# Performance work log

Hardware: AMD Instinct MI355X
Metric: run time of the kernel (lower is better)

## Reference

```python
import jax, jax.numpy as jnp
import numpy as np

B, T, H = 4, 1024, 4096
N_Q, N_KV, HD = 32, 8, 128
N_REP = N_Q // N_KV
THETA = 10000.0


def setup_inputs() -> dict:
    key = jax.random.key(0)
    k0, k1, k2 = jax.random.split(key, 3)
    x = jax.random.normal(k0, (B, T, H), dtype=jnp.float32)
    w_qkv = jax.random.normal(k1, ((N_Q + 2 * N_KV) * HD, H), dtype=jnp.float32) * 0.02
    w_proj = jax.random.normal(k2, (N_Q * HD, H), dtype=jnp.float32).T * 0.02  # [H, N_Q*HD] -> stored as [out,in]=[4096,4096]
    # real RoPE frequencies, matching precompute_freqs_cis(theta=10000)
    inv_freq = 1.0 / (THETA ** (np.arange(0, HD, 2, dtype=np.float32) / HD))  # [HD/2]
    angles = np.arange(T, dtype=np.float32)[:, None] * inv_freq[None, :]      # [T, HD/2]
    freqs_cos = jnp.asarray(np.cos(angles))
    freqs_sin = jnp.asarray(np.sin(angles))
    return {"x": x, "w_qkv": w_qkv, "w_proj": w_proj,
            "freqs_cos": freqs_cos, "freqs_sin": freqs_sin}


def _rope(x, cos, sin):
    # x: [B, T, nH, HD]; consecutive pairs (x[2i], x[2i+1]) form complex numbers
    x0 = x[..., 0::2]
    x1 = x[..., 1::2]
    c = cos[None, :, None, :]
    s = sin[None, :, None, :]
    r0 = x0 * c - x1 * s
    r1 = x0 * s + x1 * c
    return jnp.stack([r0, r1], axis=-1).reshape(x.shape)


def reference(x, w_qkv, w_proj, freqs_cos, freqs_sin):
    q_per_kv = N_Q // N_KV
    qkv = jnp.einsum('bth,oh->bto', x, w_qkv)                 # [B,T,(N_Q+2*N_KV)*HD]
    qkv = qkv.reshape(B, T, N_KV, q_per_kv + 2, HD)           # interleaved GQA layout
    q = qkv[:, :, :, :q_per_kv, :].reshape(B, T, N_Q, HD)
    k = qkv[:, :, :, q_per_kv, :]                              # [B,T,N_KV,HD]
    v = qkv[:, :, :, q_per_kv + 1, :]
    q = _rope(q, freqs_cos, freqs_sin)
    k = _rope(k, freqs_cos, freqs_sin)
    k = jnp.repeat(k, N_REP, axis=2)                           # [B,T,N_Q,HD]
    v = jnp.repeat(v, N_REP, axis=2)
    q = q.transpose(0, 2, 1, 3)                                # [B,H,T,HD]
    k = k.transpose(0, 2, 1, 3)
    v = v.transpose(0, 2, 1, 3)
    scale = 1.0 / jnp.sqrt(jnp.float32(HD))
    scores = jnp.einsum('bhqd,bhkd->bhqk', q, k) * scale       # [B,H,T,T]
    causal = jnp.tril(jnp.ones((T, T), dtype=bool))
    scores = jnp.where(causal[None, None], scores, jnp.finfo(scores.dtype).min)
    attn = jax.nn.softmax(scores, axis=-1)
    out = jnp.einsum('bhqk,bhkd->bhqd', attn, v)               # [B,H,T,HD]
    out = out.transpose(0, 2, 1, 3).reshape(B, T, N_Q * HD)
    return jnp.einsum('bto,ho->bth', out, w_proj)              # RowParallel proj, [B,T,H]
```

## Files before the change

### kernel.cpp

```cpp
#include <hip/hip_runtime.h>
#include <cstddef>

#define DEVINL __device__ __forceinline__

typedef float f32x4 __attribute__((ext_vector_type(4)));
typedef __bf16 bf16x8 __attribute__((ext_vector_type(8)));

DEVINL unsigned short f2bf(float f) {
  union { float f; unsigned int u; } v; v.f = f;
  unsigned int u = v.u;
  unsigned int r = (u + 0x7fffu + ((u >> 16) & 1u)) >> 16;
  return (unsigned short)r;
}
DEVINL float bf2f(unsigned short s) {
  union { unsigned int u; float f; } v; v.u = ((unsigned int)s) << 16;
  return v.f;
}
DEVINL uint4 pack8(const unsigned short o[8]) {
  uint4 r;
  r.x = (unsigned int)o[0] | ((unsigned int)o[1] << 16);
  r.y = (unsigned int)o[2] | ((unsigned int)o[3] << 16);
  r.z = (unsigned int)o[4] | ((unsigned int)o[5] << 16);
  r.w = (unsigned int)o[6] | ((unsigned int)o[7] << 16);
  return r;
}
DEVINL void gload16(const void* g, void* l) {
  __builtin_amdgcn_global_load_lds(
      (__attribute__((address_space(1))) void*)g,
      (__attribute__((address_space(3))) void*)l, 16, 0, 0);
}

__global__ __launch_bounds__(256) void k_cvt(const float* __restrict__ in,
                                             unsigned short* __restrict__ out, int n4) {
  int i = blockIdx.x * 256 + threadIdx.x;
  if (i >= n4) return;
  float4 v = ((const float4*)in)[i];
  ushort4 o;
  o.x = f2bf(v.x); o.y = f2bf(v.y); o.z = f2bf(v.z); o.w = f2bf(v.w);
  ((ushort4*)out)[i] = o;
}

template <int OUT_BF16>
__global__ __launch_bounds__(512, 1) void k_gemm256(const unsigned short* __restrict__ A,
                                                    const unsigned short* __restrict__ Bt,
                                                    void* __restrict__ Cout,
                                                    int M, int N, int K) {
  __shared__ __align__(16) unsigned short As[2][2][256 * 32];
  __shared__ __align__(16) unsigned short Bs[2][2][256 * 32];
  const int t = threadIdx.x, lane = t & 63;
  const int wid = t >> 6, wm = wid >> 2, wn = wid & 3;
  const int fr = lane & 15, kq = lane >> 4;
  const int nwg = gridDim.x * gridDim.y;
  int lin = blockIdx.y * gridDim.x + blockIdx.x;
  lin = (lin & 7) * (nwg >> 3) + (lin >> 3);
  const int bx = lin % gridDim.x, by = lin / gridDim.x;
  const int row0 = by * 256, col0 = bx * 256;
  const int NT = K >> 6;

  int srow[2], sgs[2];
#pragma unroll
  for (int i = 0; i < 2; ++i) {
    const int off = (i * 512 + t) * 16;
    srow[i] = off >> 6;
    sgs[i] = (((off >> 4) & 3) - (srow[i] >> 1)) & 3;
  }

#define STAGE_A(KT, KS)                                                        \
  do {                                                                         \
    const int b_ = (KT) & 1;                                                   \
    _Pragma("unroll") for (int i = 0; i < 2; ++i)                              \
        gload16(A + (size_t)(row0 + srow[i]) * K + (KT) * 64 + (KS) * 32 +     \
                    sgs[i] * 8,                                                \
                (char*)&As[b_][KS][0] + i * 8192 + wid * 1024);                \
  } while (0)
#define STAGE_B(KT, KS)                                                        \
  do {                                                                         \
    const int b_ = (KT) & 1;                                                   \
    _Pragma("unroll") for (int i = 0; i < 2; ++i)                              \
        gload16(Bt + (size_t)(col0 + srow[i]) * K + (KT) * 64 + (KS) * 32 +    \
                    sgs[i] * 8,                                                \
                (char*)&Bs[b_][KS][0] + i * 8192 + wid * 1024);                \
  } while (0)
#define LDFRAG(BUFP, ROW) \
  (*(const bf16x8*)((const char*)(BUFP) + (ROW) * 64 + ((((ROW) >> 1) + kq & 3) << 4)))

  f32x4 acc[8][4];
#pragma unroll
  for (int m = 0; m < 8; ++m)
#pragma unroll
    for (int n = 0; n < 4; ++n) acc[m][n] = f32x4{0.f, 0.f, 0.f, 0.f};

  STAGE_A(0, 0); STAGE_B(0, 0); STAGE_A(0, 1); STAGE_B(0, 1);
  STAGE_A(1, 0); STAGE_B(1, 0);
  asm volatile("s_waitcnt vmcnt(8)" ::: "memory");
  __builtin_amdgcn_s_barrier();

  for (int kt = 0; kt < NT; ++kt) {
    const unsigned short* As0 = &As[kt & 1][0][0];
    const unsigned short* As1 = &As[kt & 1][1][0];
    const unsigned short* Bs0 = &Bs[kt & 1][0][0];
    const unsigned short* Bs1 = &Bs[kt & 1][1][0];
    bf16x8 a0[4], a1[4], b0[4], b1[4];

#pragma unroll
    for (int m = 0; m < 4; ++m) a0[m] = LDFRAG(As0, wm * 128 + m * 16 + fr);
#pragma unroll
    for (int n = 0; n < 4; ++n) b0[n] = LDFRAG(Bs0, wn * 64 + n * 16 + fr);
    if (kt + 1 < NT) STAGE_A(kt + 1, 1);
    __builtin_amdgcn_sched_barrier(0);
    __builtin_amdgcn_s_barrier();
    asm volatile("s_waitcnt lgkmcnt(0)" ::: "memory");
    __builtin_amdgcn_sched_barrier(0);
    __builtin_amdgcn_s_setprio(1);
#pragma unroll
    for (int m = 0; m < 4; ++m)
#pragma unroll
      for (int n = 0; n < 4; ++n)
        acc[m][n] = __builtin_amdgcn_mfma_f32_16x16x32_bf16(a0[m], b0[n], acc[m][n], 0, 0, 0);
    __builtin_amdgcn_s_setprio(0);
    __builtin_amdgcn_s_barrier();

#pragma unroll
    for (int m = 0; m < 4; ++m) a1[m] = LDFRAG(As0, wm * 128 + 64 + m * 16 + fr);
    if (kt + 1 < NT) STAGE_B(kt + 1, 1);
    __builtin_amdgcn_sched_barrier(0);
    __builtin_amdgcn_s_barrier();
    asm volatile("s_waitcnt lgkmcnt(0)" ::: "memory");
    __builtin_amdgcn_sched_barrier(0);
    __builtin_amdgcn_s_setprio(1);
#pragma unroll
    for (int m = 0; m < 4; ++m)
#pragma unroll
      for (int n = 0; n < 4; ++n)
        acc[m + 4][n] = __builtin_amdgcn_mfma_f32_16x16x32_bf16(a1[m], b0[n], acc[m + 4][n], 0, 0, 0);
    __builtin_amdgcn_s_setprio(0);
    if (kt + 1 < NT) asm volatile("s_waitcnt vmcnt(8)" ::: "memory");
    else             asm volatile("s_waitcnt vmcnt(0)" ::: "memory");
    __builtin_amdgcn_sched_barrier(0);
    __builtin_amdgcn_s_barrier();

#pragma unroll
    for (int m = 0; m < 4; ++m) a0[m] = LDFRAG(As1, wm * 128 + m * 16 + fr);
#pragma unroll
    for (int n = 0; n < 4; ++n) b1[n] = LDFRAG(Bs1, wn * 64 + n * 16 + fr);
    if (kt + 2 < NT) STAGE_A(kt + 2, 0);
    __builtin_amdgcn_sched_barrier(0);
    __builtin_amdgcn_s_barrier();
    asm volatile("s_waitcnt lgkmcnt(0)" ::: "memory");
    __builtin_amdgcn_sched_barrier(0);
    __builtin_amdgcn_s_setprio(1);
#pragma unroll
    for (int m = 0; m < 4; ++m)
#pragma unroll
      for (int n = 0; n < 4; ++n)
        acc[m][n] = __builtin_amdgcn_mfma_f32_16x16x32_bf16(a0[m], b1[n], acc[m][n], 0, 0, 0);
    __builtin_amdgcn_s_setprio(0);
    __builtin_amdgcn_s_barrier();

#pragma unroll
    for (int m = 0; m < 4; ++m) a1[m] = LDFRAG(As1, wm * 128 + 64 + m * 16 + fr);
    if (kt + 2 < NT) STAGE_B(kt + 2, 0);
    __builtin_amdgcn_sched_barrier(0);
    __builtin_amdgcn_s_barrier();
    asm volatile("s_waitcnt lgkmcnt(0)" ::: "memory");
    __builtin_amdgcn_sched_barrier(0);
    __builtin_amdgcn_s_setprio(1);
#pragma unroll
    for (int m = 0; m < 4; ++m)
#pragma unroll
      for (int n = 0; n < 4; ++n)
        acc[m + 4][n] = __builtin_amdgcn_mfma_f32_16x16x32_bf16(a1[m], b1[n], acc[m + 4][n], 0, 0, 0);
    __builtin_amdgcn_s_setprio(0);
    if (kt + 2 < NT)      asm volatile("s_waitcnt vmcnt(8)" ::: "memory");
    else if (kt + 1 < NT) asm volatile("s_waitcnt vmcnt(4)" ::: "memory");
    __builtin_amdgcn_sched_barrier(0);
    __builtin_amdgcn_s_barrier();
  }
#undef STAGE_A
#undef STAGE_B
#undef LDFRAG

  const int rsub = kq * 4;
#pragma unroll
  for (int m = 0; m < 8; ++m)
#pragma unroll
    for (int n = 0; n < 4; ++n)
#pragma unroll
      for (int r = 0; r < 4; ++r) {
        const size_t row = (size_t)row0 + wm * 128 + m * 16 + rsub + r;
        const size_t col = (size_t)col0 + wn * 64 + n * 16 + fr;
        if (OUT_BF16)
          ((unsigned short*)Cout)[row * N + col] = f2bf(acc[m][n][r]);
        else
          ((float*)Cout)[row * N + col] = acc[m][n][r];
      }
}

__global__ __launch_bounds__(256) void k_rope(const unsigned short* __restrict__ qkv,
                                              const float* __restrict__ fcos,
                                              const float* __restrict__ fsin,
                                              unsigned short* __restrict__ Qb,
                                              unsigned short* __restrict__ Kb) {
  const int idx = blockIdx.x * 256 + threadIdx.x;
  if (idx >= 4096 * 640) return;
  const int bt = idx / 640;
  const int r = idx - bt * 640;
  const int g = r / 80;
  const int rr = r - g * 80;
  const int slot = rr >> 4;
  const int d0 = (rr & 15) * 8;
  const int o0 = g * 768 + slot * 128 + d0;
  const int b = bt >> 10, tt = bt & 1023;

  uint4 raw = *(const uint4*)&qkv[(size_t)bt * 6144 + o0];
  unsigned short us[8] = {
      (unsigned short)(raw.x & 0xffff), (unsigned short)(raw.x >> 16),
      (unsigned short)(raw.y & 0xffff), (unsigned short)(raw.y >> 16),
      (unsigned short)(raw.z & 0xffff), (unsigned short)(raw.z >> 16),
      (unsigned short)(raw.w & 0xffff), (unsigned short)(raw.w >> 16)};

  float4 c = *(const float4*)&fcos[tt * 64 + (d0 >> 1)];
  float4 s = *(const float4*)&fsin[tt * 64 + (d0 >> 1)];
  const float sc = (slot < 4) ? 0.08838834764831845f : 1.0f;
  float cj[4] = {c.x, c.y, c.z, c.w};
  float sj[4] = {s.x, s.y, s.z, s.w};
  unsigned short os[8];
#pragma unroll
  for (int j = 0; j < 4; ++j) {
    float x0 = bf2f(us[2 * j]), x1 = bf2f(us[2 * j + 1]);
    os[2 * j] = f2bf((x0 * cj[j] - x1 * sj[j]) * sc);
    os[2 * j + 1] = f2bf((x0 * sj[j] + x1 * cj[j]) * sc);
  }
  if (slot < 4) {
    const int h = g * 4 + slot;
    *(uint4*)&Qb[((size_t)(b * 32 + h) * 1024 + tt) * 128 + d0] = pack8(os);
  } else {
    *(uint4*)&Kb[((size_t)(b * 8 + g) * 1024 + tt) * 128 + d0] = pack8(os);
  }
}

__global__ __launch_bounds__(256) void k_vtrans(const unsigned short* __restrict__ qkv,
                                                unsigned short* __restrict__ VT) {
  const int t = threadIdx.x;
  const int tt0 = blockIdx.x * 128;
  const int bg = blockIdx.y;
  const int b = bg >> 3, g = bg & 7;
  const int tj = t & 15;
  const int ti = t >> 4;
  union U4 { uint4 v; unsigned int u[4]; };
  U4 in[8], out[8];
  const unsigned short* src =
      qkv + (size_t)(b * 1024 + tt0 + ti * 8) * 6144 + g * 768 + 640 + tj * 8;
#pragma unroll
  for (int r = 0; r < 8; ++r) in[r].v = *(const uint4*)(src + (size_t)r * 6144);
#pragma unroll
  for (int c = 0; c < 8; ++c) {
    const unsigned int sel = (c & 1) ? 0x07060302u : 0x05040100u;
    const int dw = c >> 1;
#pragma unroll
    for (int w = 0; w < 4; ++w)
      out[c].u[w] = __builtin_amdgcn_perm(in[2 * w + 1].u[dw], in[2 * w].u[dw], sel);
  }
  unsigned short* dst = VT + (size_t)bg * 131072 + (size_t)(tj * 8) * 1024 + tt0 + ti * 8;
#pragma unroll
  for (int c = 0; c < 8; ++c) *(uint4*)(dst + (size_t)c * 1024) = out[c].v;
}

__global__ __launch_bounds__(512, 1) void k_attn(const unsigned short* __restrict__ Qb,
                                                 const unsigned short* __restrict__ Kb,
                                                 const unsigned short* __restrict__ VT,
                                                 unsigned short* __restrict__ AO) {
  __shared__ __align__(16) unsigned short Ks[2][64 * 128];
  __shared__ __align__(16) unsigned short Vt[2][128 * 64];
  __shared__ __align__(16) unsigned short Ps[8][32 * 64];
  const int t = threadIdx.x, lane = t & 63, wid = t >> 6;
  const int hh = wid >> 1, qh = wid & 1;
  const int bg = blockIdx.x, b = bg >> 3, g = bg & 7;
  const int qi = 15 - (int)blockIdx.y;
  const int q0 = qi * 64;
  const int h = g * 4 + hh;
  const int fr = lane & 15, kq = lane >> 4;
  const size_t kvbase = (size_t)bg * (1024 * 128);
  const size_t vtbase = (size_t)bg * (128 * 1024);

#define ASTAGE(TILE, BUF)                                                      \
  do {                                                                         \
    const int kv0_ = (TILE) * 64;                                              \
    _Pragma("unroll") for (int it = 0; it < 2; ++it) {                         \
      const int off = it * 8192 + t * 16;                                      \
      const int r_ = off >> 8, cb_ = off & 255;                                \
      const int scb_ = cb_ ^ ((r_ & 7) << 4);                                  \
      gload16(Kb + kvbase + (size_t)(kv0_ + r_) * 128 + (scb_ >> 1),           \
              (char*)Ks[BUF] + off);                                           \
    }                                                                          \
    _Pragma("unroll") for (int it = 0; it < 2; ++it) {                         \
      const int off = it * 8192 + t * 16;                                      \
      const int rd_ = off >> 7, cb_ = off & 127;                               \
      const int scb_ = cb_ ^ ((rd_ & 7) << 4);                                 \
      gload16(VT + vtbase + (size_t)rd_ * 1024 + kv0_ + (scb_ >> 1),           \
              (char*)Vt[BUF] + off);                                           \
    }                                                                          \
  } while (0)

  bf16x8 qf[2][4];
  {
    const unsigned short* Qp0 = Qb + ((size_t)(b * 32 + h) * 1024 + q0 + qh * 32) * 128;
#pragma unroll
    for (int qr = 0; qr < 2; ++qr)
#pragma unroll
      for (int ks = 0; ks < 4; ++ks)
        qf[qr][ks] = *(const bf16x8*)&Qp0[(size_t)(qr * 16 + fr) * 128 + ks * 32 + kq * 8];
  }
  float mrow[2][4], lrow[2][4];
#pragma unroll
  for (int qr = 0; qr < 2; ++qr)
#pragma unroll
    for (int rg = 0; rg < 4; ++rg) { mrow[qr][rg] = -1e30f; lrow[qr][rg] = 0.f; }
  f32x4 of[2][8];
#pragma unroll
  for (int qr = 0; qr < 2; ++qr)
#pragma unroll
    for (int n = 0; n < 8; ++n) of[qr][n] = f32x4{0.f, 0.f, 0.f, 0.f};

  const int ntiles = qi + 1;
  ASTAGE(0, 0);

  for (int kt = 0; kt < ntiles; ++kt) {
    const int buf = kt & 1;
    const int kv0 = kt * 64;
    if (kt + 1 < ntiles) {
      ASTAGE(kt + 1, buf ^ 1);
      asm volatile("s_waitcnt vmcnt(4)" ::: "memory");
    } else {
      asm volatile("s_waitcnt vmcnt(0)" ::: "memory");
    }
    __builtin_amdgcn_s_barrier();
    __builtin_amdgcn_sched_barrier(0);

    f32x4 sacc[2][4];
#pragma unroll
    for (int qr = 0; qr < 2; ++qr)
#pragma unroll
      for (int n = 0; n < 4; ++n) sacc[qr][n] = f32x4{0.f, 0.f, 0.f, 0.f};
#pragma unroll
    for (int n = 0; n < 4; ++n) {
      const int row = n * 16 + fr;
      const int sw = (row & 7) << 4;
      bf16x8 kf[4];
#pragma unroll
      for (int ks = 0; ks < 4; ++ks)
        kf[ks] = *(const bf16x8*)((const char*)Ks[buf] + row * 256 + ((ks * 64 + kq * 16) ^ sw));
      __builtin_amdgcn_s_setprio(1);
#pragma unroll
      for (int qr = 0; qr < 2; ++qr)
#pragma unroll
        for (int ks = 0; ks < 4; ++ks)
          sacc[qr][n] =
              __builtin_amdgcn_mfma_f32_16x16x32_bf16(qf[qr][ks], kf[ks], sacc[qr][n], 0, 0, 0);
      __builtin_amdgcn_s_setprio(0);
    }

#pragma unroll
    for (int qr = 0; qr < 2; ++qr)
#pragma unroll
      for (int rg = 0; rg < 4; ++rg) {
        const int qrow = q0 + qh * 32 + qr * 16 + kq * 4 + rg;
        float s[4];
#pragma unroll
        for (int n = 0; n < 4; ++n) {
          s[n] = sacc[qr][n][rg];
          if (kv0 + n * 16 + fr > qrow) s[n] = -1e30f;
        }
        float mx = fmaxf(fmaxf(s[0], s[1]), fmaxf(s[2], s[3]));
#pragma unroll
        for (int o = 1; o < 16; o <<= 1) mx = fmaxf(mx, __shfl_xor(mx, o));
        const float mnew = fmaxf(mrow[qr][rg], mx);
        float p[4];
#pragma unroll
        for (int n = 0; n < 4; ++n) p[n] = __expf(s[n] - mnew);
        float sum = (p[0] + p[1]) + (p[2] + p[3]);
#pragma unroll
        for (int o = 1; o < 16; o <<= 1) sum += __shfl_xor(sum, o);
        const float fac = __expf(mrow[qr][rg] - mnew);
        lrow[qr][rg] = lrow[qr][rg] * fac + sum;
        mrow[qr][rg] = mnew;
#pragma unroll
        for (int n = 0; n < 8; ++n) of[qr][n][rg] *= fac;
        const int q = qr * 16 + kq * 4 + rg;
        const int swp = (q & 7) << 4;
#pragma unroll
        for (int n = 0; n < 4; ++n)
          *(unsigned short*)((char*)Ps[wid] + q * 128 + ((2 * (n * 16 + fr)) ^ swp)) =
              f2bf(p[n]);
      }
    asm volatile("s_waitcnt lgkmcnt(0)" ::: "memory");
    __builtin_amdgcn_sched_barrier(0);

    bf16x8 pa[2][2];
#pragma unroll
    for (int qr = 0; qr < 2; ++qr) {
      const int prow = qr * 16 + fr;
      const int swp = (prow & 7) << 4;
#pragma unroll
      for (int kk = 0; kk < 2; ++kk)
        pa[qr][kk] = *(const bf16x8*)((const char*)Ps[wid] + prow * 128 +
                                      ((kk * 64 + kq * 16) ^ swp));
    }
#pragma unroll
    for (int n = 0; n < 8; ++n) {
      const int row = n * 16 + fr;
      const int sw = (row & 7) << 4;
      bf16x8 vf[2];
#pragma unroll
      for (int kk = 0; kk < 2; ++kk)
        vf[kk] = *(const bf16x8*)((const char*)Vt[buf] + row * 128 + ((kk * 64 + kq * 16) ^ sw));
      __builtin_amdgcn_s_setprio(1);
#pragma unroll
      for (int qr = 0; qr < 2; ++qr)
#pragma unroll
        for (int kk = 0; kk < 2; ++kk)
          of[qr][n] = __builtin_amdgcn_mfma_f32_16x16x32_bf16(pa[qr][kk], vf[kk], of[qr][n], 0, 0, 0);
      __builtin_amdgcn_s_setprio(0);
    }
    asm volatile("s_waitcnt lgkmcnt(0)" ::: "memory");
    __builtin_amdgcn_sched_barrier(0);
    __builtin_amdgcn_s_barrier();
  }
#undef ASTAGE

  float inv[2][4];
#pragma unroll
  for (int qr = 0; qr < 2; ++qr)
#pragma unroll
    for (int rg = 0; rg < 4; ++rg) inv[qr][rg] = 1.0f / lrow[qr][rg];
#pragma unroll
  for (int qr = 0; qr < 2; ++qr)
#pragma unroll
    for (int n = 0; n < 8; ++n)
#pragma unroll
      for (int rg = 0; rg < 4; ++rg) {
        const size_t row = (size_t)b * 1024 + q0 + qh * 32 + qr * 16 + kq * 4 + rg;
        const size_t col = (size_t)h * 128 + n * 16 + fr;
        AO[row * 4096 + col] = f2bf(of[qr][n][rg] * inv[qr][rg]);
      }
}

extern "C" void kernel_launch(void* const* d_in, const int* in_sizes, int n_in,
                              void* d_out, int out_size, void* d_ws, size_t ws_size,
                              hipStream_t stream) {
  const float* x = (const float*)d_in[0];
  const float* w_qkv = (const float*)d_in[1];
  const float* w_proj = (const float*)d_in[2];
  const float* fcos = (const float*)d_in[3];
  const float* fsin = (const float*)d_in[4];
  float* out = (float*)d_out;

  char* ws = (char*)d_ws;
  unsigned short* XB    = (unsigned short*)(ws + 0);
  unsigned short* WQKVB = (unsigned short*)(ws + 33554432);
  unsigned short* QKVB  = (unsigned short*)(ws + 83886080);
  unsigned short* QB    = (unsigned short*)(ws + 134217728);
  unsigned short* KB    = (unsigned short*)(ws + 167772160);
  unsigned short* VTB   = (unsigned short*)(ws + 176160768);
  unsigned short* WPROJB = XB;
  unsigned short* AOB    = QKVB;

  k_cvt<<<16384, 256, 0, stream>>>(x, XB, 4194304);
  k_cvt<<<24576, 256, 0, stream>>>(w_qkv, WQKVB, 6291456);
  k_gemm256<1><<<dim3(24, 16), 512, 0, stream>>>(XB, WQKVB, QKVB, 4096, 6144, 4096);
  k_cvt<<<16384, 256, 0, stream>>>(w_proj, WPROJB, 4194304);
  k_rope<<<10240, 256, 0, stream>>>(QKVB, fcos, fsin, QB, KB);
  k_vtrans<<<dim3(8, 32), 256, 0, stream>>>(QKVB, VTB);
  k_attn<<<dim3(32, 16), 512, 0, stream>>>(QB, KB, VTB, AOB);
  k_gemm256<0><<<dim3(16, 16), 512, 0, stream>>>(AOB, WPROJB, out, 4096, 4096, 4096);
}
```

Baseline: 512.3 us.

## Templatize GEMM tile width and use 256x128 tiles for output projection

The GEMM kernel is templated on tile width and warp layout. The output projection now uses 256x128 tiles on a 32x16 grid (512 workgroups instead of 256), to fill the 256 CUs better, and launch bounds drop the one-block-per-CU hint. The K pipeline is also simplified from two 32-wide sub-stages per 64-wide step to a double buffer over 32-wide steps, with a full vmcnt(0) wait each iteration. That wait lowers load/compute overlap and adds barriers per K unit, which may slow the QKV GEMM.

```diff
diff --git a/kernel.cpp b/kernel.cpp
--- a/kernel.cpp
+++ b/kernel.cpp
@@ -40,22 +40,27 @@
   ((ushort4*)out)[i] = o;
 }
 
-template <int OUT_BF16>
-__global__ __launch_bounds__(512, 1) void k_gemm256(const unsigned short* __restrict__ A,
-                                                    const unsigned short* __restrict__ Bt,
-                                                    void* __restrict__ Cout,
-                                                    int M, int N, int K) {
-  __shared__ __align__(16) unsigned short As[2][2][256 * 32];
-  __shared__ __align__(16) unsigned short Bs[2][2][256 * 32];
+template <int OUT_BF16, int BN, int WM, int WN>
+__global__ __launch_bounds__(512) void k_gemm(const unsigned short* __restrict__ A,
+                                              const unsigned short* __restrict__ Bt,
+                                              void* __restrict__ Cout,
+                                              int M, int N, int K) {
+  constexpr int MRW = 256 / WM;
+  constexpr int NRW = BN / WN;
+  constexpr int MR = MRW / 16;
+  constexpr int NR = NRW / 16;
+  constexpr int BI = (BN == 256) ? 2 : 1;
+  __shared__ __align__(16) unsigned short As[2][256 * 32];
+  __shared__ __align__(16) unsigned short Bs[2][BN * 32];
   const int t = threadIdx.x, lane = t & 63;
-  const int wid = t >> 6, wm = wid >> 2, wn = wid & 3;
+  const int wid = t >> 6, wm = wid / WN, wn = wid % WN;
   const int fr = lane & 15, kq = lane >> 4;
   const int nwg = gridDim.x * gridDim.y;
   int lin = blockIdx.y * gridDim.x + blockIdx.x;
   lin = (lin & 7) * (nwg >> 3) + (lin >> 3);
   const int bx = lin % gridDim.x, by = lin / gridDim.x;
-  const int row0 = by * 256, col0 = bx * 256;
-  const int NT = K >> 6;
+  const int row0 = by * 256, col0 = bx * BN;
+  const int NT = K >> 5;
 
   int srow[2], sgs[2];
 #pragma unroll
@@ -65,48 +70,45 @@
     sgs[i] = (((off >> 4) & 3) - (srow[i] >> 1)) & 3;
   }
 
-#define STAGE_A(KT, KS)                                                        \
+#define STAGE_A(KT, BUF)                                                       \
   do {                                                                         \
-    const int b_ = (KT) & 1;                                                   \
     _Pragma("unroll") for (int i = 0; i < 2; ++i)                              \
-        gload16(A + (size_t)(row0 + srow[i]) * K + (KT) * 64 + (KS) * 32 +     \
-                    sgs[i] * 8,                                                \
-                (char*)&As[b_][KS][0] + i * 8192 + wid * 1024);                \
+        gload16(A + (size_t)(row0 + srow[i]) * K + (KT) * 32 + sgs[i] * 8,     \
+                (char*)&As[BUF][0] + i * 8192 + wid * 1024);                   \
   } while (0)
-#define STAGE_B(KT, KS)                                                        \
+#define STAGE_B(KT, BUF)                                                       \
   do {                                                                         \
-    const int b_ = (KT) & 1;                                                   \
-    _Pragma("unroll") for (int i = 0; i < 2; ++i)                              \
-        gload16(Bt + (size_t)(col0 + srow[i]) * K + (KT) * 64 + (KS) * 32 +    \
-                    sgs[i] * 8,                                                \
-                (char*)&Bs[b_][KS][0] + i * 8192 + wid * 1024);                \
+    _Pragma("unroll") for (int i = 0; i < BI; ++i)                             \
+        gload16(Bt + (size_t)(col0 + srow[i]) * K + (KT) * 32 + sgs[i] * 8,    \
+                (char*)&Bs[BUF][0] + i * 8192 + wid * 1024);                   \
   } while (0)
 #define LDFRAG(BUFP, ROW) \
   (*(const bf16x8*)((const char*)(BUFP) + (ROW) * 64 + ((((ROW) >> 1) + kq & 3) << 4)))
 
-  f32x4 acc[8][4];
-#pragma unroll
-  for (int m = 0; m < 8; ++m)
-#pragma unroll
-    for (int n = 0; n < 4; ++n) acc[m][n] = f32x4{0.f, 0.f, 0.f, 0.f};
-
-  STAGE_A(0, 0); STAGE_B(0, 0); STAGE_A(0, 1); STAGE_B(0, 1);
-  STAGE_A(1, 0); STAGE_B(1, 0);
-  asm volatile("s_waitcnt vmcnt(8)" ::: "memory");
+  f32x4 acc[MR][NR];
+#pragma unroll
+  for (int m = 0; m < MR; ++m)
+#pragma unroll
+    for (int n = 0; n < NR; ++n) acc[m][n] = f32x4{0.f, 0.f, 0.f, 0.f};
+
+  STAGE_A(0, 0); STAGE_B(0, 0);
+  asm volatile("s_waitcnt vmcnt(0)" ::: "memory");
   __builtin_amdgcn_s_barrier();
 
   for (int kt = 0; kt < NT; ++kt) {
-    const unsigned short* As0 = &As[kt & 1][0][0];
-    const unsigned short* As1 = &As[kt & 1][1][0];
-    const unsigned short* Bs0 = &Bs[kt & 1][0][0];
-    const unsigned short* Bs1 = &Bs[kt & 1][1][0];
-    bf16x8 a0[4], a1[4], b0[4], b1[4];
-
-#pragma unroll
-    for (int m = 0; m < 4; ++m) a0[m] = LDFRAG(As0, wm * 128 + m * 16 + fr);
-#pragma unroll
-    for (int n = 0; n < 4; ++n) b0[n] = LDFRAG(Bs0, wn * 64 + n * 16 + fr);
-    if (kt + 1 < NT) STAGE_A(kt + 1, 1);
+    const int buf = kt & 1;
+    const unsigned short* Ap = &As[buf][0];
+    const unsigned short* Bp = &Bs[buf][0];
+    bf16x8 af[4], bfr[NR];
+
+#pragma unroll
+    for (int m = 0; m < 4; ++m) af[m] = LDFRAG(Ap, wm * MRW + m * 16 + fr);
+#pragma unroll
+    for (int n = 0; n < NR; ++n) bfr[n] = LDFRAG(Bp, wn * NRW + n * 16 + fr);
+    if (kt + 1 < NT) {
+      STAGE_A(kt + 1, buf ^ 1);
+      if (MR == 4) STAGE_B(kt + 1, buf ^ 1);
+    }
     __builtin_amdgcn_sched_barrier(0);
     __builtin_amdgcn_s_barrier();
     asm volatile("s_waitcnt lgkmcnt(0)" ::: "memory");
@@ -115,64 +117,30 @@
 #pragma unroll
     for (int m = 0; m < 4; ++m)
 #pragma unroll
-      for (int n = 0; n < 4; ++n)
-        acc[m][n] = __builtin_amdgcn_mfma_f32_16x16x32_bf16(a0[m], b0[n], acc[m][n], 0, 0, 0);
+      for (int n = 0; n < NR; ++n)
+        acc[m][n] = __builtin_amdgcn_mfma_f32_16x16x32_bf16(af[m], bfr[n], acc[m][n], 0, 0, 0);
     __builtin_amdgcn_s_setprio(0);
-    __builtin_amdgcn_s_barrier();
-
-#pragma unroll
-    for (int m = 0; m < 4; ++m) a1[m] = LDFRAG(As0, wm * 128 + 64 + m * 16 + fr);
-    if (kt + 1 < NT) STAGE_B(kt + 1, 1);
-    __builtin_amdgcn_sched_barrier(0);
-    __builtin_amdgcn_s_barrier();
-    asm volatile("s_waitcnt lgkmcnt(0)" ::: "memory");
-    __builtin_amdgcn_sched_barrier(0);
-    __builtin_amdgcn_s_setprio(1);
-#pragma unroll
-    for (int m = 0; m < 4; ++m)
-#pragma unroll
-      for (int n = 0; n < 4; ++n)
-        acc[m + 4][n] = __builtin_amdgcn_mfma_f32_16x16x32_bf16(a1[m], b0[n], acc[m + 4][n], 0, 0, 0);
-    __builtin_amdgcn_s_setprio(0);
-    if (kt + 1 < NT) asm volatile("s_waitcnt vmcnt(8)" ::: "memory");
-    else             asm volatile("s_waitcnt vmcnt(0)" ::: "memory");
-    __builtin_amdgcn_sched_barrier(0);
-    __builtin_amdgcn_s_barrier();
-
-#pragma unroll
-    for (int m = 0; m < 4; ++m) a0[m] = LDFRAG(As1, wm * 128 + m * 16 + fr);
-#pragma unroll
-    for (int n = 0; n < 4; ++n) b1[n] = LDFRAG(Bs1, wn * 64 + n * 16 + fr);
-    if (kt + 2 < NT) STAGE_A(kt + 2, 0);
-    __builtin_amdgcn_sched_barrier(0);
-    __builtin_amdgcn_s_barrier();
-    asm volatile("s_waitcnt lgkmcnt(0)" ::: "memory");
-    __builtin_amdgcn_sched_barrier(0);
-    __builtin_amdgcn_s_setprio(1);
-#pragma unroll
-    for (int m = 0; m < 4; ++m)
-#pragma unroll
-      for (int n = 0; n < 4; ++n)
-        acc[m][n] = __builtin_amdgcn_mfma_f32_16x16x32_bf16(a0[m], b1[n], acc[m][n], 0, 0, 0);
-    __builtin_amdgcn_s_setprio(0);
-    __builtin_amdgcn_s_barrier();
-
-#pragma unroll
-    for (int m = 0; m < 4; ++m) a1[m] = LDFRAG(As1, wm * 128 + 64 + m * 16 + fr);
-    if (kt + 2 < NT) STAGE_B(kt + 2, 0);
-    __builtin_amdgcn_sched_barrier(0);
-    __builtin_amdgcn_s_barrier();
-    asm volatile("s_waitcnt lgkmcnt(0)" ::: "memory");
-    __builtin_amdgcn_sched_barrier(0);
-    __builtin_amdgcn_s_setprio(1);
-#pragma unroll
-    for (int m = 0; m < 4; ++m)
-#pragma unroll
-      for (int n = 0; n < 4; ++n)
-        acc[m + 4][n] = __builtin_amdgcn_mfma_f32_16x16x32_bf16(a1[m], b1[n], acc[m + 4][n], 0, 0, 0);
-    __builtin_amdgcn_s_setprio(0);
-    if (kt + 2 < NT)      asm volatile("s_waitcnt vmcnt(8)" ::: "memory");
-    else if (kt + 1 < NT) asm volatile("s_waitcnt vmcnt(4)" ::: "memory");
+
+    if constexpr (MR == 8) {
+      __builtin_amdgcn_s_barrier();
+      bf16x8 a1[4];
+#pragma unroll
+      for (int m = 0; m < 4; ++m) a1[m] = LDFRAG(Ap, wm * MRW + 64 + m * 16 + fr);
+      if (kt + 1 < NT) STAGE_B(kt + 1, buf ^ 1);
+      __builtin_amdgcn_sched_barrier(0);
+      __builtin_amdgcn_s_barrier();
+      asm volatile("s_waitcnt lgkmcnt(0)" ::: "memory");
+      __builtin_amdgcn_sched_barrier(0);
+      __builtin_amdgcn_s_setprio(1);
+#pragma unroll
+      for (int m = 0; m < 4; ++m)
+#pragma unroll
+        for (int n = 0; n < NR; ++n)
+          acc[m + 4][n] =
+              __builtin_amdgcn_mfma_f32_16x16x32_bf16(a1[m], bfr[n], acc[m + 4][n], 0, 0, 0);
+      __builtin_amdgcn_s_setprio(0);
+    }
+    asm volatile("s_waitcnt vmcnt(0) lgkmcnt(0)" ::: "memory");
     __builtin_amdgcn_sched_barrier(0);
     __builtin_amdgcn_s_barrier();
   }
@@ -182,13 +150,13 @@
 
   const int rsub = kq * 4;
 #pragma unroll
-  for (int m = 0; m < 8; ++m)
-#pragma unroll
-    for (int n = 0; n < 4; ++n)
+  for (int m = 0; m < MR; ++m)
+#pragma unroll
+    for (int n = 0; n < NR; ++n)
 #pragma unroll
       for (int r = 0; r < 4; ++r) {
-        const size_t row = (size_t)row0 + wm * 128 + m * 16 + rsub + r;
-        const size_t col = (size_t)col0 + wn * 64 + n * 16 + fr;
+        const size_t row = (size_t)row0 + wm * MRW + m * 16 + rsub + r;
+        const size_t col = (size_t)col0 + wn * NRW + n * 16 + fr;
         if (OUT_BF16)
           ((unsigned short*)Cout)[row * N + col] = f2bf(acc[m][n][r]);
         else
@@ -467,10 +435,10 @@
 
   k_cvt<<<16384, 256, 0, stream>>>(x, XB, 4194304);
   k_cvt<<<24576, 256, 0, stream>>>(w_qkv, WQKVB, 6291456);
-  k_gemm256<1><<<dim3(24, 16), 512, 0, stream>>>(XB, WQKVB, QKVB, 4096, 6144, 4096);
+  k_gemm<1, 256, 2, 4><<<dim3(24, 16), 512, 0, stream>>>(XB, WQKVB, QKVB, 4096, 6144, 4096);
   k_cvt<<<16384, 256, 0, stream>>>(w_proj, WPROJB, 4194304);
   k_rope<<<10240, 256, 0, stream>>>(QKVB, fcos, fsin, QB, KB);
   k_vtrans<<<dim3(8, 32), 256, 0, stream>>>(QKVB, VTB);
   k_attn<<<dim3(32, 16), 512, 0, stream>>>(QB, KB, VTB, AOB);
-  k_gemm256<0><<<dim3(16, 16), 512, 0, stream>>>(AOB, WPROJB, out, 4096, 4096, 4096);
-}
+  k_gemm<0, 128, 4, 2><<<dim3(32, 16), 512, 0, stream>>>(AOB, WPROJB, out, 4096, 4096, 4096);
+}
```

Measured after the change: 525.2 us. 2.5% more time.
